# Optimization experiments

Hardware: AMD Instinct MI355X
Metric: run time of the kernel (lower is better)

Reference implementation:

```python
import jax, jax.numpy as jnp
import numpy as np

C = 128
ATTN_DIM = C // 8   # 16
VALUE_DIM = C // 2  # 64

def _xavier(key, shape):
    # xavier_uniform for torch Linear weight (out,in); we store transposed (in,out)
    fan_in, fan_out = shape[0], shape[1]
    a = jnp.sqrt(6.0 / (fan_in + fan_out))
    return jax.random.uniform(key, shape, jnp.float32, -a, a)

def setup_inputs() -> dict:
    key = jax.random.key(0)
    ks = jax.random.split(key, 5)
    x = jax.random.normal(ks[0], (8, C, 64, 64), jnp.float32)
    return {
        "x": x,
        "Wq": _xavier(ks[1], (C, ATTN_DIM)),  "bq": jnp.zeros((ATTN_DIM,), jnp.float32),
        "Wk": _xavier(ks[2], (C, ATTN_DIM)),  "bk": jnp.zeros((ATTN_DIM,), jnp.float32),
        "Wv": _xavier(ks[3], (C, VALUE_DIM)), "bv": jnp.zeros((VALUE_DIM,), jnp.float32),
        "Wo": _xavier(ks[4], (VALUE_DIM, C)), "bo": jnp.zeros((C,), jnp.float32),
        "gamma": jnp.ones((), jnp.float32),
    }

def _maxpool2x2(t):
    # t: (N, D, H, W) -> (N, D, H//2, W//2), MaxPool2d((2,2), stride=2)
    N, D, H, W = t.shape
    return t.reshape(N, D, H // 2, 2, W // 2, 2).max(axis=(3, 5))

def reference(x, Wq, bq, Wk, bk, Wv, bv, Wo, bo, gamma):
    N, Cc, H, W = x.shape
    xf = x.reshape(N, Cc, H * W).transpose(0, 2, 1)          # (N, HW, C)
    q = xf @ Wq + bq                                          # (N, HW, d)
    k = (xf @ Wk + bk).reshape(N, H, W, ATTN_DIM).transpose(0, 3, 1, 2)
    k = _maxpool2x2(k).reshape(N, ATTN_DIM, -1)               # (N, d, HW/4)
    scores = jnp.einsum('bqd,bdk->bqk', q, k)                 # (N, HW, HW/4)
    attn = jax.nn.softmax(scores, axis=-1)
    v = (xf @ Wv + bv).reshape(N, H, W, VALUE_DIM).transpose(0, 3, 1, 2)
    v = _maxpool2x2(v).reshape(N, VALUE_DIM, -1).transpose(0, 2, 1)  # (N, HW/4, dv)
    ao = jnp.einsum('bqk,bkv->bqv', attn, v)                  # (N, HW, dv)
    out = (ao @ Wo + bo).reshape(N, H, W, Cc).transpose(0, 3, 1, 2)
    return x + gamma * out
```

## Files before the change

kernel.cpp:

```cpp
#include <hip/hip_runtime.h>
#include <hip/hip_bf16.h>
#include <cstddef>
#include <cstdint>

#define CC   128
#define AD   16
#define VD   64
#define HWN  4096
#define PJ   1024
#define NB   8

typedef short short8 __attribute__((ext_vector_type(8)));
typedef float f32x4  __attribute__((ext_vector_type(4)));
typedef unsigned short u16;

__device__ inline u16 f2bf(float f) {
    __hip_bfloat16 h = __float2bfloat16(f);
    union { __hip_bfloat16 h; u16 u; } c; c.h = h; return c.u;
}
__device__ inline unsigned pk2(float a, float b) {
    __hip_bfloat162 h = __float22bfloat162_rn(make_float2(a, b));
    union { __hip_bfloat162 h; unsigned u; } c; c.h = h; return c.u;
}
__device__ inline float bf16f(u16 v) {
    union { unsigned u; float f; } a; a.u = ((unsigned)v) << 16;
    return a.f;
}

__device__ inline int ph128(int r, int c) { return r * 128 + ((((c >> 3) ^ (r & 7)) << 3) | (c & 7)); }
__device__ inline int ph64 (int r, int c) { return r * 64  + ((((c >> 3) ^ (r & 7)) << 3) | (c & 7)); }

__device__ inline void stage16(const u16* g, u16* l) {
#if __has_builtin(__builtin_amdgcn_global_load_lds)
    __builtin_amdgcn_global_load_lds(
        (const __attribute__((address_space(1))) unsigned int*)g,
        (__attribute__((address_space(3))) unsigned int*)l, 16, 0, 0);
#else
    *(uint4*)l = *(const uint4*)g;
#endif
}

__global__ __launch_bounds__(256) void k_proj(
    const float* __restrict__ x,
    const float* __restrict__ Wq, const float* __restrict__ bq,
    const float* __restrict__ Wk, const float* __restrict__ bk,
    const float* __restrict__ Wv, const float* __restrict__ bv,
    u16* __restrict__ Qp, u16* __restrict__ Kp, u16* __restrict__ Vt2)
{
    __shared__ __align__(16) u16 xT[128 * 128];
    __shared__ __align__(16) u16 WT[96 * 128];

    const int tile = blockIdx.x, n = blockIdx.y, t = threadIdx.x;
    const int p0 = tile * 128;
    const int l = t & 63, w = t >> 6, g = l >> 4, lm = l & 15;

    {
        const float* xb = x + (size_t)n * CC * HWN + p0;
#pragma unroll
        for (int it = 0; it < 4; ++it) {
            const int idx = t + 256 * it;
            const int p4 = idx & 31, c4 = idx >> 5;
            const float* bp = xb + p4 * 4;
            const f32x4 r0 = *(const f32x4*)(bp + (size_t)(c4 * 4 + 0) * HWN);
            const f32x4 r1 = *(const f32x4*)(bp + (size_t)(c4 * 4 + 1) * HWN);
            const f32x4 r2 = *(const f32x4*)(bp + (size_t)(c4 * 4 + 2) * HWN);
            const f32x4 r3 = *(const f32x4*)(bp + (size_t)(c4 * 4 + 3) * HWN);
#pragma unroll
            for (int pp = 0; pp < 4; ++pp) {
                const int pos = p4 * 4 + pp;
                uint2 v;
                v.x = pk2(r0[pp], r1[pp]);
                v.y = pk2(r2[pp], r3[pp]);
                *(uint2*)&xT[pos * 128 + ((((c4 >> 1) ^ (pos & 7)) << 3) | ((c4 & 1) * 4))] = v;
            }
        }
    }
#pragma unroll
    for (int it = 0; it < 2; ++it) {
        const int idx = t + 256 * it;
        const int d4 = idx & 3, ch = idx >> 2;
        float4 v = *(const float4*)(Wq + ch * AD + d4 * 4);
        WT[ph128(d4 * 4 + 0, ch)] = f2bf(v.x);
        WT[ph128(d4 * 4 + 1, ch)] = f2bf(v.y);
        WT[ph128(d4 * 4 + 2, ch)] = f2bf(v.z);
        WT[ph128(d4 * 4 + 3, ch)] = f2bf(v.w);
        v = *(const float4*)(Wk + ch * AD + d4 * 4);
        WT[ph128(16 + d4 * 4 + 0, ch)] = f2bf(v.x);
        WT[ph128(16 + d4 * 4 + 1, ch)] = f2bf(v.y);
        WT[ph128(16 + d4 * 4 + 2, ch)] = f2bf(v.z);
        WT[ph128(16 + d4 * 4 + 3, ch)] = f2bf(v.w);
    }
#pragma unroll
    for (int it = 0; it < 8; ++it) {
        const int idx = t + 256 * it;
        const int d4 = idx & 15, ch = idx >> 4;
        const float4 v = *(const float4*)(Wv + ch * VD + d4 * 4);
        WT[ph128(32 + d4 * 4 + 0, ch)] = f2bf(v.x);
        WT[ph128(32 + d4 * 4 + 1, ch)] = f2bf(v.y);
        WT[ph128(32 + d4 * 4 + 2, ch)] = f2bf(v.z);
        WT[ph128(32 + d4 * 4 + 3, ch)] = f2bf(v.w);
    }
    __syncthreads();

    f32x4 acc[2][6];
#pragma unroll
    for (int i = 0; i < 2; ++i)
#pragma unroll
        for (int j = 0; j < 6; ++j) acc[i][j] = (f32x4){0.f, 0.f, 0.f, 0.f};
#pragma unroll
    for (int ks = 0; ks < 4; ++ks) {
        const short8 a0 = *(const short8*)&xT[ph128(w * 16 + lm,       ks * 32 + g * 8)];
        const short8 a1 = *(const short8*)&xT[ph128((w + 4) * 16 + lm, ks * 32 + g * 8)];
#pragma unroll
        for (int nt = 0; nt < 6; ++nt) {
            const short8 b = *(const short8*)&WT[ph128(nt * 16 + lm, ks * 32 + g * 8)];
            acc[0][nt] = __builtin_amdgcn_mfma_f32_16x16x32_bf16(a0, b, acc[0][nt], 0, 0, 0);
            acc[1][nt] = __builtin_amdgcn_mfma_f32_16x16x32_bf16(a1, b, acc[1][nt], 0, 0, 0);
        }
    }

    const float bqv = bq[lm], bkv = bk[lm];

#pragma unroll
    for (int mi = 0; mi < 2; ++mi) {
        const int mt = w + mi * 4;
#pragma unroll
        for (int r = 0; r < 4; ++r) {
            const int pos = mt * 16 + g * 4 + r;
            Qp[((size_t)n * HWN + p0 + pos) * AD + lm] = f2bf(acc[mi][0][r] + bqv);
        }
    }
#pragma unroll
    for (int a = 0; a < 2; ++a) {
        const float m = fmaxf(fmaxf(acc[0][1][2 * a], acc[0][1][2 * a + 1]),
                              fmaxf(acc[1][1][2 * a], acc[1][1][2 * a + 1])) + bkv;
        const int j = tile * 32 + w * 8 + g * 2 + a;
        const int dsw = (((lm >> 3) ^ (j & 1)) << 3) | (lm & 7);
        Kp[((size_t)n * PJ + j) * AD + dsw] = f2bf(m);
    }
#pragma unroll
    for (int nt = 0; nt < 4; ++nt) {
        const int dv = nt * 16 + lm;
        const float bvv = bv[dv];
        const float m0 = fmaxf(fmaxf(acc[0][nt + 2][0], acc[0][nt + 2][1]),
                               fmaxf(acc[1][nt + 2][0], acc[1][nt + 2][1])) + bvv;
        const float m1 = fmaxf(fmaxf(acc[0][nt + 2][2], acc[0][nt + 2][3]),
                               fmaxf(acc[1][nt + 2][2], acc[1][nt + 2][3])) + bvv;
        const int jl  = (tile & 3) * 32 + w * 8 + g * 2;
        const int jsw = (((jl >> 3) ^ (dv & 7)) << 3) | (jl & 7);
        *(unsigned*)&Vt2[((((size_t)n * 8 + (tile >> 2)) * VD + dv) << 7) + jsw] = pk2(m0, m1);
    }
}

__global__ __launch_bounds__(256) void k_attn(
    const float* __restrict__ x,
    const u16* __restrict__ Qp, const u16* __restrict__ Kp, const u16* __restrict__ Vt2,
    const float* __restrict__ Wo, const float* __restrict__ bo,
    const float* __restrict__ gma,
    float* __restrict__ out)
{
    __shared__ __align__(16) u16 KV[2][10240];
    __shared__ __align__(16) u16 PB[4 * 2048];

    const int n = blockIdx.y, t = threadIdx.x;
    const int q0b = blockIdx.x * 64;
    const int l = t & 63, w = t >> 6, g = l >> 4, lm = l & 15;

    short8 qf = {0, 0, 0, 0, 0, 0, 0, 0};
    if (g < 2)
        qf = *(const short8*)(Qp + ((size_t)n * HWN + q0b + w * 16 + lm) * AD + g * 8);

    float xr[8][4];
#pragma unroll
    for (int mt = 0; mt < 8; ++mt)
#pragma unroll
        for (int r = 0; r < 4; ++r)
            xr[mt][r] = x[((size_t)n * CC + mt * 16 + g * 4 + r) * HWN + q0b + w * 16 + lm];

    const u16* Kg = Kp  + (size_t)n * PJ * AD;
    const u16* Vg = Vt2 + (size_t)n * 8 * VD * 128;

    {
        stage16(Kg + t * 8, &KV[0][t * 8]);
#pragma unroll
        for (int i = 0; i < 4; ++i)
            stage16(Vg + ((w * 4 + i) * 64 + l) * 8, &KV[0][2048 + (w * 4 + i) * 512 + l * 8]);
    }
    __syncthreads();

    f32x4 O[4];
#pragma unroll
    for (int i = 0; i < 4; ++i) O[i] = (f32x4){0.f, 0.f, 0.f, 0.f};
    float mr[4] = {-1e30f, -1e30f, -1e30f, -1e30f};
    float lr[4] = {0.f, 0.f, 0.f, 0.f};
    u16* Pl = PB + w * 2048;

    for (int ch = 0; ch < 8; ++ch) {
        const u16* Kl = KV[ch & 1];
        const u16* Vl = KV[ch & 1] + 2048;

        if (ch < 7) {
            const int b = (ch + 1) & 1;
            const size_t ko = (size_t)(ch + 1) * 2048, vo = (size_t)(ch + 1) * 8192;
            stage16(Kg + ko + t * 8, &KV[b][t * 8]);
#pragma unroll
            for (int i = 0; i < 4; ++i)
                stage16(Vg + vo + ((w * 4 + i) * 64 + l) * 8,
                        &KV[b][2048 + (w * 4 + i) * 512 + l * 8]);
        }

        f32x4 S[8];
#pragma unroll
        for (int jt = 0; jt < 8; ++jt) {
            short8 kb = {0, 0, 0, 0, 0, 0, 0, 0};
            if (g < 2) {
                const int j = jt * 16 + lm;
                kb = *(const short8*)&Kl[(j * 2 + (g ^ (j & 1))) * 8];
            }
            const f32x4 z = (f32x4){0.f, 0.f, 0.f, 0.f};
            S[jt] = __builtin_amdgcn_mfma_f32_16x16x32_bf16(qf, kb, z, 0, 0, 0);
        }

#pragma unroll
        for (int r = 0; r < 4; ++r) {
            float cm = S[0][r];
#pragma unroll
            for (int jt = 1; jt < 8; ++jt) cm = fmaxf(cm, S[jt][r]);
            cm = fmaxf(cm, __shfl_xor(cm, 1));
            cm = fmaxf(cm, __shfl_xor(cm, 2));
            cm = fmaxf(cm, __shfl_xor(cm, 4));
            cm = fmaxf(cm, __shfl_xor(cm, 8));
            const float nm = fmaxf(mr[r], cm);
            const float al = __expf(mr[r] - nm);
            mr[r] = nm;
            const int row = g * 4 + r;
            float sum = 0.f;
#pragma unroll
            for (int jt = 0; jt < 8; ++jt) {
                const float p = __expf(S[jt][r] - nm);
                sum += p;
                Pl[ph128(row, jt * 16 + lm)] = f2bf(p);
            }
            sum += __shfl_xor(sum, 1);
            sum += __shfl_xor(sum, 2);
            sum += __shfl_xor(sum, 4);
            sum += __shfl_xor(sum, 8);
            lr[r] = lr[r] * al + sum;
            O[0][r] *= al; O[1][r] *= al; O[2][r] *= al; O[3][r] *= al;
        }

#pragma unroll
        for (int ks = 0; ks < 4; ++ks) {
            const short8 pf = *(const short8*)&Pl[ph128(lm, ks * 32 + g * 8)];
#pragma unroll
            for (int dt = 0; dt < 4; ++dt) {
                const short8 vf = *(const short8*)&Vl[ph128(dt * 16 + lm, ks * 32 + g * 8)];
                O[dt] = __builtin_amdgcn_mfma_f32_16x16x32_bf16(pf, vf, O[dt], 0, 0, 0);
            }
        }
        __syncthreads();
    }

    u16* Ol = Pl;
#pragma unroll
    for (int r = 0; r < 4; ++r) {
        const float inv = 1.f / lr[r];
        const int row = g * 4 + r;
#pragma unroll
        for (int dt = 0; dt < 4; ++dt)
            Ol[ph64(row, dt * 16 + lm)] = f2bf(O[dt][r] * inv);
    }
    u16* WoTl = (u16*)KV;
#pragma unroll
    for (int it = 0; it < 8; ++it) {
        const int idx = t + 256 * it;
        const int c4 = idx & 31, dv = idx >> 5;
        const float4 v = *(const float4*)(Wo + dv * CC + c4 * 4);
        WoTl[ph64(c4 * 4 + 0, dv)] = f2bf(v.x);
        WoTl[ph64(c4 * 4 + 1, dv)] = f2bf(v.y);
        WoTl[ph64(c4 * 4 + 2, dv)] = f2bf(v.z);
        WoTl[ph64(c4 * 4 + 3, dv)] = f2bf(v.w);
    }
    __syncthreads();

    const float gm = gma[0];
#pragma unroll
    for (int mt = 0; mt < 8; ++mt) {
        f32x4 D = (f32x4){0.f, 0.f, 0.f, 0.f};
#pragma unroll
        for (int ks = 0; ks < 2; ++ks) {
            const short8 af = *(const short8*)&WoTl[ph64(mt * 16 + lm, ks * 32 + g * 8)];
            const short8 bf = *(const short8*)&Ol[ph64(lm, ks * 32 + g * 8)];
            D = __builtin_amdgcn_mfma_f32_16x16x32_bf16(af, bf, D, 0, 0, 0);
        }
#pragma unroll
        for (int r = 0; r < 4; ++r) {
            const int c = mt * 16 + g * 4 + r;
            const size_t off = ((size_t)n * CC + c) * HWN + q0b + w * 16 + lm;
            out[off] = xr[mt][r] + gm * (D[r] + bo[c]);
        }
    }
}

extern "C" void kernel_launch(void* const* d_in, const int* in_sizes, int n_in,
                              void* d_out, int out_size, void* d_ws, size_t ws_size,
                              hipStream_t stream) {
    const float* x     = (const float*)d_in[0];
    const float* Wq    = (const float*)d_in[1];
    const float* bq    = (const float*)d_in[2];
    const float* Wk    = (const float*)d_in[3];
    const float* bk    = (const float*)d_in[4];
    const float* Wv    = (const float*)d_in[5];
    const float* bv    = (const float*)d_in[6];
    const float* Wo    = (const float*)d_in[7];
    const float* bo    = (const float*)d_in[8];
    const float* gamma = (const float*)d_in[9];
    float* out = (float*)d_out;

    u16* Qp  = (u16*)d_ws;
    u16* Kp  = Qp + (size_t)NB * HWN * AD;
    u16* Vt2 = Kp + (size_t)NB * PJ * AD;

    k_proj<<<dim3(32, NB), 256, 0, stream>>>(x, Wq, bq, Wk, bk, Wv, bv, Qp, Kp, Vt2);
    k_attn<<<dim3(64, NB), 256, 0, stream>>>(x, Qp, Kp, Vt2, Wo, bo, gamma, out);
}
```

Measured before the change: 122.0 us.

## Split projection over z, drop attention double buffering, cut register and LDS use

The projection kernel now uses a third grid dimension, so each block handles 64 positions instead of 128, which halves its xT LDS tile. Its four waves are split into position and output-column groups. The K/V global layout changes: Vt becomes plain row-major and the swizzle moves into the staging load addresses. In the attention kernel the double-buffered K/V LDS is replaced by a single buffer with a sync per chunk, and the residual x values are loaded at the epilogue instead of held in 32 registers. Both kernels get a launch_bounds minimum of 4 blocks to raise occupancy, at the cost of losing the overlap of next-chunk loads with compute.

```diff
diff --git a/kernel.cpp b/kernel.cpp
--- a/kernel.cpp
+++ b/kernel.cpp
@@ -1,7 +1,6 @@
 #include <hip/hip_runtime.h>
 #include <hip/hip_bf16.h>
 #include <cstddef>
-#include <cstdint>
 
 #define CC   128
 #define AD   16
@@ -21,10 +20,6 @@
 __device__ inline unsigned pk2(float a, float b) {
     __hip_bfloat162 h = __float22bfloat162_rn(make_float2(a, b));
     union { __hip_bfloat162 h; unsigned u; } c; c.h = h; return c.u;
-}
-__device__ inline float bf16f(u16 v) {
-    union { unsigned u; float f; } a; a.u = ((unsigned)v) << 16;
-    return a.f;
 }
 
 __device__ inline int ph128(int r, int c) { return r * 128 + ((((c >> 3) ^ (r & 7)) << 3) | (c & 7)); }
@@ -40,38 +35,39 @@
 #endif
 }
 
-__global__ __launch_bounds__(256) void k_proj(
+__global__ __launch_bounds__(256, 4) void k_proj(
     const float* __restrict__ x,
     const float* __restrict__ Wq, const float* __restrict__ bq,
     const float* __restrict__ Wk, const float* __restrict__ bk,
     const float* __restrict__ Wv, const float* __restrict__ bv,
-    u16* __restrict__ Qp, u16* __restrict__ Kp, u16* __restrict__ Vt2)
+    u16* __restrict__ Qp, u16* __restrict__ Kp, u16* __restrict__ Vt)
 {
-    __shared__ __align__(16) u16 xT[128 * 128];
+    __shared__ __align__(16) u16 xT[64 * 128];
     __shared__ __align__(16) u16 WT[96 * 128];
 
-    const int tile = blockIdx.x, n = blockIdx.y, t = threadIdx.x;
+    const int tile = blockIdx.x, n = blockIdx.y, z = blockIdx.z, t = threadIdx.x;
+    const int l = t & 63, w = t >> 6, g = l >> 4, lm = l & 15;
     const int p0 = tile * 128;
-    const int l = t & 63, w = t >> 6, g = l >> 4, lm = l & 15;
 
     {
-        const float* xb = x + (size_t)n * CC * HWN + p0;
-#pragma unroll
-        for (int it = 0; it < 4; ++it) {
+        const float* xb = x + (size_t)n * CC * HWN + p0 + z * 32;
+#pragma unroll
+        for (int it = 0; it < 2; ++it) {
             const int idx = t + 256 * it;
-            const int p4 = idx & 31, c4 = idx >> 5;
-            const float* bp = xb + p4 * 4;
+            const int p4 = idx & 15, c4 = idx >> 4;
+            const int gofs = (p4 & 7) * 4 + (p4 >> 3) * 64;
+            const float* bp = xb + gofs;
             const f32x4 r0 = *(const f32x4*)(bp + (size_t)(c4 * 4 + 0) * HWN);
             const f32x4 r1 = *(const f32x4*)(bp + (size_t)(c4 * 4 + 1) * HWN);
             const f32x4 r2 = *(const f32x4*)(bp + (size_t)(c4 * 4 + 2) * HWN);
             const f32x4 r3 = *(const f32x4*)(bp + (size_t)(c4 * 4 + 3) * HWN);
 #pragma unroll
             for (int pp = 0; pp < 4; ++pp) {
-                const int pos = p4 * 4 + pp;
+                const int lp = p4 * 4 + pp;
                 uint2 v;
                 v.x = pk2(r0[pp], r1[pp]);
                 v.y = pk2(r2[pp], r3[pp]);
-                *(uint2*)&xT[pos * 128 + ((((c4 >> 1) ^ (pos & 7)) << 3) | ((c4 & 1) * 4))] = v;
+                *(uint2*)&xT[lp * 128 + ((((c4 >> 1) ^ (lp & 7)) << 3) | ((c4 & 1) * 4))] = v;
             }
         }
     }
@@ -102,64 +98,71 @@
     }
     __syncthreads();
 
-    f32x4 acc[2][6];
+    const int pw = w & 1, ng = w >> 1;
+    f32x4 acc[2][3];
 #pragma unroll
     for (int i = 0; i < 2; ++i)
 #pragma unroll
-        for (int j = 0; j < 6; ++j) acc[i][j] = (f32x4){0.f, 0.f, 0.f, 0.f};
+        for (int j = 0; j < 3; ++j) acc[i][j] = (f32x4){0.f, 0.f, 0.f, 0.f};
 #pragma unroll
     for (int ks = 0; ks < 4; ++ks) {
-        const short8 a0 = *(const short8*)&xT[ph128(w * 16 + lm,       ks * 32 + g * 8)];
-        const short8 a1 = *(const short8*)&xT[ph128((w + 4) * 16 + lm, ks * 32 + g * 8)];
-#pragma unroll
-        for (int nt = 0; nt < 6; ++nt) {
-            const short8 b = *(const short8*)&WT[ph128(nt * 16 + lm, ks * 32 + g * 8)];
-            acc[0][nt] = __builtin_amdgcn_mfma_f32_16x16x32_bf16(a0, b, acc[0][nt], 0, 0, 0);
-            acc[1][nt] = __builtin_amdgcn_mfma_f32_16x16x32_bf16(a1, b, acc[1][nt], 0, 0, 0);
-        }
-    }
-
-    const float bqv = bq[lm], bkv = bk[lm];
-
-#pragma unroll
-    for (int mi = 0; mi < 2; ++mi) {
-        const int mt = w + mi * 4;
-#pragma unroll
-        for (int r = 0; r < 4; ++r) {
-            const int pos = mt * 16 + g * 4 + r;
-            Qp[((size_t)n * HWN + p0 + pos) * AD + lm] = f2bf(acc[mi][0][r] + bqv);
-        }
-    }
-#pragma unroll
-    for (int a = 0; a < 2; ++a) {
-        const float m = fmaxf(fmaxf(acc[0][1][2 * a], acc[0][1][2 * a + 1]),
-                              fmaxf(acc[1][1][2 * a], acc[1][1][2 * a + 1])) + bkv;
-        const int j = tile * 32 + w * 8 + g * 2 + a;
-        const int dsw = (((lm >> 3) ^ (j & 1)) << 3) | (lm & 7);
-        Kp[((size_t)n * PJ + j) * AD + dsw] = f2bf(m);
-    }
-#pragma unroll
-    for (int nt = 0; nt < 4; ++nt) {
-        const int dv = nt * 16 + lm;
-        const float bvv = bv[dv];
-        const float m0 = fmaxf(fmaxf(acc[0][nt + 2][0], acc[0][nt + 2][1]),
-                               fmaxf(acc[1][nt + 2][0], acc[1][nt + 2][1])) + bvv;
-        const float m1 = fmaxf(fmaxf(acc[0][nt + 2][2], acc[0][nt + 2][3]),
-                               fmaxf(acc[1][nt + 2][2], acc[1][nt + 2][3])) + bvv;
-        const int jl  = (tile & 3) * 32 + w * 8 + g * 2;
-        const int jsw = (((jl >> 3) ^ (dv & 7)) << 3) | (jl & 7);
-        *(unsigned*)&Vt2[((((size_t)n * 8 + (tile >> 2)) * VD + dv) << 7) + jsw] = pk2(m0, m1);
-    }
-}
-
-__global__ __launch_bounds__(256) void k_attn(
+        const short8 a0 = *(const short8*)&xT[ph128(pw * 16 + lm,      ks * 32 + g * 8)];
+        const short8 a1 = *(const short8*)&xT[ph128(32 + pw * 16 + lm, ks * 32 + g * 8)];
+#pragma unroll
+        for (int j = 0; j < 3; ++j) {
+            const short8 b = *(const short8*)&WT[ph128((ng * 3 + j) * 16 + lm, ks * 32 + g * 8)];
+            acc[0][j] = __builtin_amdgcn_mfma_f32_16x16x32_bf16(a0, b, acc[0][j], 0, 0, 0);
+            acc[1][j] = __builtin_amdgcn_mfma_f32_16x16x32_bf16(a1, b, acc[1][j], 0, 0, 0);
+        }
+    }
+
+    const int pbase = p0 + z * 32 + pw * 16 + g * 4;
+    const int jp = tile * 32 + z * 16 + pw * 8 + g * 2;
+
+    if (ng == 0) {
+        const float bqv = bq[lm];
+#pragma unroll
+        for (int mi = 0; mi < 2; ++mi)
+#pragma unroll
+            for (int r = 0; r < 4; ++r)
+                Qp[((size_t)n * HWN + pbase + mi * 64 + r) * AD + lm] = f2bf(acc[mi][0][r] + bqv);
+        const float bkv = bk[lm];
+#pragma unroll
+        for (int a = 0; a < 2; ++a) {
+            const float m = fmaxf(fmaxf(acc[0][1][2 * a], acc[0][1][2 * a + 1]),
+                                  fmaxf(acc[1][1][2 * a], acc[1][1][2 * a + 1])) + bkv;
+            Kp[((size_t)n * PJ + jp + a) * AD + lm] = f2bf(m);
+        }
+        {
+            const float bvv = bv[lm];
+            const float m0 = fmaxf(fmaxf(acc[0][2][0], acc[0][2][1]),
+                                   fmaxf(acc[1][2][0], acc[1][2][1])) + bvv;
+            const float m1 = fmaxf(fmaxf(acc[0][2][2], acc[0][2][3]),
+                                   fmaxf(acc[1][2][2], acc[1][2][3])) + bvv;
+            *(unsigned*)&Vt[((size_t)n * VD + lm) * PJ + jp] = pk2(m0, m1);
+        }
+    } else {
+#pragma unroll
+        for (int j = 0; j < 3; ++j) {
+            const int dv = (j + 1) * 16 + lm;
+            const float bvv = bv[dv];
+            const float m0 = fmaxf(fmaxf(acc[0][j][0], acc[0][j][1]),
+                                   fmaxf(acc[1][j][0], acc[1][j][1])) + bvv;
+            const float m1 = fmaxf(fmaxf(acc[0][j][2], acc[0][j][3]),
+                                   fmaxf(acc[1][j][2], acc[1][j][3])) + bvv;
+            *(unsigned*)&Vt[((size_t)n * VD + dv) * PJ + jp] = pk2(m0, m1);
+        }
+    }
+}
+
+__global__ __launch_bounds__(256, 4) void k_attn(
     const float* __restrict__ x,
-    const u16* __restrict__ Qp, const u16* __restrict__ Kp, const u16* __restrict__ Vt2,
+    const u16* __restrict__ Qp, const u16* __restrict__ Kp, const u16* __restrict__ Vt,
     const float* __restrict__ Wo, const float* __restrict__ bo,
     const float* __restrict__ gma,
     float* __restrict__ out)
 {
-    __shared__ __align__(16) u16 KV[2][10240];
+    __shared__ __align__(16) u16 KVl[10240];
     __shared__ __align__(16) u16 PB[4 * 2048];
 
     const int n = blockIdx.y, t = threadIdx.x;
@@ -170,44 +173,30 @@
     if (g < 2)
         qf = *(const short8*)(Qp + ((size_t)n * HWN + q0b + w * 16 + lm) * AD + g * 8);
 
-    float xr[8][4];
-#pragma unroll
-    for (int mt = 0; mt < 8; ++mt)
-#pragma unroll
-        for (int r = 0; r < 4; ++r)
-            xr[mt][r] = x[((size_t)n * CC + mt * 16 + g * 4 + r) * HWN + q0b + w * 16 + lm];
-
-    const u16* Kg = Kp  + (size_t)n * PJ * AD;
-    const u16* Vg = Vt2 + (size_t)n * 8 * VD * 128;
-
-    {
-        stage16(Kg + t * 8, &KV[0][t * 8]);
-#pragma unroll
-        for (int i = 0; i < 4; ++i)
-            stage16(Vg + ((w * 4 + i) * 64 + l) * 8, &KV[0][2048 + (w * 4 + i) * 512 + l * 8]);
-    }
-    __syncthreads();
+    const u16* Kg = Kp + (size_t)n * PJ * AD
+                  + (size_t)(t >> 1) * AD + ((t & 1) ^ ((t >> 1) & 1)) * 8;
+    const int vdv0 = (w * 4) * 4 + (l >> 4);
+    const u16* Vg0 = Vt + ((size_t)n * VD) * PJ;
+
+    u16* Vl = KVl + 2048;
+    u16* Pl = PB + w * 2048;
 
     f32x4 O[4];
 #pragma unroll
     for (int i = 0; i < 4; ++i) O[i] = (f32x4){0.f, 0.f, 0.f, 0.f};
     float mr[4] = {-1e30f, -1e30f, -1e30f, -1e30f};
     float lr[4] = {0.f, 0.f, 0.f, 0.f};
-    u16* Pl = PB + w * 2048;
 
     for (int ch = 0; ch < 8; ++ch) {
-        const u16* Kl = KV[ch & 1];
-        const u16* Vl = KV[ch & 1] + 2048;
-
-        if (ch < 7) {
-            const int b = (ch + 1) & 1;
-            const size_t ko = (size_t)(ch + 1) * 2048, vo = (size_t)(ch + 1) * 8192;
-            stage16(Kg + ko + t * 8, &KV[b][t * 8]);
-#pragma unroll
-            for (int i = 0; i < 4; ++i)
-                stage16(Vg + vo + ((w * 4 + i) * 64 + l) * 8,
-                        &KV[b][2048 + (w * 4 + i) * 512 + l * 8]);
-        }
+        const int j0 = ch * 128;
+        stage16(Kg + (size_t)j0 * AD, &KVl[t * 8]);
+#pragma unroll
+        for (int i = 0; i < 4; ++i) {
+            const int dv = vdv0 + i * 4;
+            stage16(Vg0 + (size_t)dv * PJ + j0 + (((l & 15) ^ (dv & 7)) * 8),
+                    &Vl[(w * 4 + i) * 512 + l * 8]);
+        }
+        __syncthreads();
 
         f32x4 S[8];
 #pragma unroll
@@ -215,7 +204,7 @@
             short8 kb = {0, 0, 0, 0, 0, 0, 0, 0};
             if (g < 2) {
                 const int j = jt * 16 + lm;
-                kb = *(const short8*)&Kl[(j * 2 + (g ^ (j & 1))) * 8];
+                kb = *(const short8*)&KVl[(j * 2 + (g ^ (j & 1))) * 8];
             }
             const f32x4 z = (f32x4){0.f, 0.f, 0.f, 0.f};
             S[jt] = __builtin_amdgcn_mfma_f32_16x16x32_bf16(qf, kb, z, 0, 0, 0);
@@ -270,34 +259,36 @@
         for (int dt = 0; dt < 4; ++dt)
             Ol[ph64(row, dt * 16 + lm)] = f2bf(O[dt][r] * inv);
     }
-    u16* WoTl = (u16*)KV;
 #pragma unroll
     for (int it = 0; it < 8; ++it) {
         const int idx = t + 256 * it;
         const int c4 = idx & 31, dv = idx >> 5;
         const float4 v = *(const float4*)(Wo + dv * CC + c4 * 4);
-        WoTl[ph64(c4 * 4 + 0, dv)] = f2bf(v.x);
-        WoTl[ph64(c4 * 4 + 1, dv)] = f2bf(v.y);
-        WoTl[ph64(c4 * 4 + 2, dv)] = f2bf(v.z);
-        WoTl[ph64(c4 * 4 + 3, dv)] = f2bf(v.w);
+        KVl[ph64(c4 * 4 + 0, dv)] = f2bf(v.x);
+        KVl[ph64(c4 * 4 + 1, dv)] = f2bf(v.y);
+        KVl[ph64(c4 * 4 + 2, dv)] = f2bf(v.z);
+        KVl[ph64(c4 * 4 + 3, dv)] = f2bf(v.w);
     }
     __syncthreads();
 
     const float gm = gma[0];
 #pragma unroll
     for (int mt = 0; mt < 8; ++mt) {
+        float xr[4];
+        const size_t obase = ((size_t)n * CC + mt * 16 + g * 4) * HWN + q0b + w * 16 + lm;
+#pragma unroll
+        for (int r = 0; r < 4; ++r) xr[r] = x[obase + (size_t)r * HWN];
         f32x4 D = (f32x4){0.f, 0.f, 0.f, 0.f};
 #pragma unroll
         for (int ks = 0; ks < 2; ++ks) {
-            const short8 af = *(const short8*)&WoTl[ph64(mt * 16 + lm, ks * 32 + g * 8)];
+            const short8 af = *(const short8*)&KVl[ph64(mt * 16 + lm, ks * 32 + g * 8)];
             const short8 bf = *(const short8*)&Ol[ph64(lm, ks * 32 + g * 8)];
             D = __builtin_amdgcn_mfma_f32_16x16x32_bf16(af, bf, D, 0, 0, 0);
         }
 #pragma unroll
         for (int r = 0; r < 4; ++r) {
             const int c = mt * 16 + g * 4 + r;
-            const size_t off = ((size_t)n * CC + c) * HWN + q0b + w * 16 + lm;
-            out[off] = xr[mt][r] + gm * (D[r] + bo[c]);
+            out[obase + (size_t)r * HWN] = xr[r] + gm * (D[r] + bo[c]);
         }
     }
 }
@@ -317,10 +308,10 @@
     const float* gamma = (const float*)d_in[9];
     float* out = (float*)d_out;
 
-    u16* Qp  = (u16*)d_ws;
-    u16* Kp  = Qp + (size_t)NB * HWN * AD;
-    u16* Vt2 = Kp + (size_t)NB * PJ * AD;
-
-    k_proj<<<dim3(32, NB), 256, 0, stream>>>(x, Wq, bq, Wk, bk, Wv, bv, Qp, Kp, Vt2);
-    k_attn<<<dim3(64, NB), 256, 0, stream>>>(x, Qp, Kp, Vt2, Wo, bo, gamma, out);
-}
+    u16* Qp = (u16*)d_ws;
+    u16* Kp = Qp + (size_t)NB * HWN * AD;
+    u16* Vt = Kp + (size_t)NB * PJ * AD;
+
+    k_proj<<<dim3(32, NB, 2), 256, 0, stream>>>(x, Wq, bq, Wk, bk, Wv, bv, Qp, Kp, Vt);
+    k_attn<<<dim3(64, NB), 256, 0, stream>>>(x, Qp, Kp, Vt, Wo, bo, gamma, out);
+}
```

Result: slower. 124.7 us (+2.2%).
